# Optimization experiments

Measured on AMD Instinct MI355X. Metric: run time of the kernel, lower is better.

## Reference

```python
import jax, jax.numpy as jnp
import numpy as np

EPS = 1e-5
SCALE = 2
K_UP = 5


def _conv(x, w, pad):
    return jax.lax.conv_general_dilated(
        x, w, window_strides=(1, 1), padding=[(pad, pad), (pad, pad)],
        dimension_numbers=("NCHW", "OIHW", "NCHW"))


def _bn(x, gamma, beta, mean, var):
    scale = gamma / jnp.sqrt(var + EPS)
    return x * scale[None, :, None, None] + (beta - mean * scale)[None, :, None, None]


def _pixel_shuffle(x, r):
    b, cr2, h, w = x.shape
    c = cr2 // (r * r)
    x = x.reshape(b, c, r, r, h, w)
    x = x.transpose(0, 1, 4, 2, 5, 3)  # b, c, h, r, w, r
    return x.reshape(b, c, h * r, w * r)


def setup_inputs() -> dict:
    key = jax.random.key(0)
    ks = jax.random.split(key, 6)
    c, c_mid, k_enc = 256, 64, 3
    n_k = (SCALE * K_UP) ** 2  # 100
    return {
        "x": jax.random.normal(ks[0], (2, c, 64, 64), jnp.float32),
        "comp_w": jax.random.normal(ks[1], (c_mid, c, 1, 1), jnp.float32) * 0.05,
        "comp_gamma": jnp.ones((c_mid,), jnp.float32),
        "comp_beta": jnp.zeros((c_mid,), jnp.float32),
        "comp_mean": jax.random.normal(ks[2], (c_mid,), jnp.float32) * 0.1,
        "comp_var": jax.random.uniform(ks[3], (c_mid,), jnp.float32, 0.5, 1.5),
        "enc_w": jax.random.normal(ks[4], (n_k, c_mid, k_enc, k_enc), jnp.float32) * 0.05,
        "enc_gamma": jnp.ones((n_k,), jnp.float32),
        "enc_beta": jnp.zeros((n_k,), jnp.float32),
        "enc_mean": jax.random.normal(ks[5], (n_k,), jnp.float32) * 0.1,
        "enc_var": jnp.ones((n_k,), jnp.float32),
    }


def reference(x, comp_w, comp_gamma, comp_beta, comp_mean, comp_var,
              enc_w, enc_gamma, enc_beta, enc_mean, enc_var):
    b, c, h, w = x.shape
    h_, w_ = h * SCALE, w * SCALE
    # comp: 1x1 conv -> BN -> ReLU
    W = jax.nn.relu(_bn(_conv(x, comp_w, 0), comp_gamma, comp_beta, comp_mean, comp_var))
    # enc: 3x3 conv -> BN (no relu)
    W = _bn(_conv(W, enc_w, 1), enc_gamma, enc_beta, enc_mean, enc_var)
    # pixel shuffle to [b, k_up^2, h_, w_] then softmax over kernel dim
    W = _pixel_shuffle(W, SCALE)
    W = jax.nn.softmax(W, axis=1)
    # nearest upsample x2
    Xu = jnp.repeat(jnp.repeat(x, SCALE, axis=2), SCALE, axis=3)
    # unfold: kernel k_up, dilation=SCALE, padding=k_up//2*SCALE
    pad = (K_UP // 2) * SCALE
    Xp = jnp.pad(Xu, ((0, 0), (0, 0), (pad, pad), (pad, pad)))
    patches = jnp.stack(
        [Xp[:, :, i * SCALE:i * SCALE + h_, j * SCALE:j * SCALE + w_]
         for i in range(K_UP) for j in range(K_UP)], axis=2)  # [b,c,k^2,h_,w_]
    return jnp.einsum("bkhw,bckhw->bchw", W, patches)
```

## Files before the change

### kernel.cpp

```cpp
#include <hip/hip_runtime.h>
#include <hip/hip_bf16.h>

typedef __hip_bfloat16 bf16;
#define EPSF 1e-5f

__global__ void k1_comp(const float* __restrict__ x, const float* __restrict__ w,
                        const float* __restrict__ gamma, const float* __restrict__ beta,
                        const float* __restrict__ mean, const float* __restrict__ var,
                        float* __restrict__ comp) {
    __shared__ float shx[2][32 * 64];
    __shared__ float shw[256 * 20];
    const int pxt = blockIdx.x;
    const int ocg = blockIdx.y;
    const int b   = blockIdx.z;
    const int tid  = threadIdx.x;
    const int wave = tid >> 6, lane = tid & 63;
    const int oc0l = wave * 4;
    const int px0 = pxt << 6;
    const float* xb = x + b * (256 * 4096) + px0;

    const int f40 = tid * 2, f41 = tid * 2 + 1;
    const int r0 = f40 >> 4, c0 = f40 & 15;
    const int r1 = f41 >> 4, c1 = f41 & 15;

    float wtmp[16];
    #pragma unroll
    for (int k = 0; k < 16; ++k)
        wtmp[k] = w[(ocg * 16 + k) * 256 + tid];
    float4 xa = *(const float4*)(xb + r0 * 4096 + c0 * 4);
    float4 xc = *(const float4*)(xb + r1 * 4096 + c1 * 4);

    #pragma unroll
    for (int k = 0; k < 16; ++k)
        shw[tid * 20 + k] = wtmp[k];
    *(float4*)(&shx[0][r0 * 64 + c0 * 4]) = xa;
    *(float4*)(&shx[0][r1 * 64 + c1 * 4]) = xc;
    __syncthreads();

    float acc[4] = {0.f, 0.f, 0.f, 0.f};

    for (int icc = 0; icc < 8; ++icc) {
        const int buf = icc & 1;
        float4 na, nc;
        if (icc < 7) {
            na = *(const float4*)(xb + ((icc + 1) * 32 + r0) * 4096 + c0 * 4);
            nc = *(const float4*)(xb + ((icc + 1) * 32 + r1) * 4096 + c1 * 4);
        }
        #pragma unroll 8
        for (int ic_l = 0; ic_l < 32; ++ic_l) {
            float xv = shx[buf][ic_l * 64 + lane];
            float4 wv = *(const float4*)(&shw[(icc * 32 + ic_l) * 20 + oc0l]);
            acc[0] += xv * wv.x;
            acc[1] += xv * wv.y;
            acc[2] += xv * wv.z;
            acc[3] += xv * wv.w;
        }
        if (icc < 7) {
            *(float4*)(&shx[buf ^ 1][r0 * 64 + c0 * 4]) = na;
            *(float4*)(&shx[buf ^ 1][r1 * 64 + c1 * 4]) = nc;
        }
        __syncthreads();
    }
    #pragma unroll
    for (int m = 0; m < 4; ++m) {
        int mo = ocg * 16 + oc0l + m;
        float s = gamma[mo] * rsqrtf(var[mo] + EPSF);
        float r = acc[m] * s + (beta[mo] - mean[mo] * s);
        comp[(b * 64 + mo) * 4096 + px0 + lane] = fmaxf(r, 0.f);
    }
}

__global__ void k2_enc_part(const float* __restrict__ comp, const float* __restrict__ w,
                            float* __restrict__ encp) {
    __shared__ float sh[8 * 660];
    const int tile = blockIdx.x;
    const int og   = blockIdx.y >> 2;
    const int icc  = blockIdx.y & 3;
    const int b    = blockIdx.z;
    const int ty0 = tile << 3;
    const int tid = threadIdx.x;
    const int tx = tid & 31, ty = tid >> 5;
    const int o0 = og * 5;

    float accA[5], accB[5];
    #pragma unroll
    for (int i = 0; i < 5; ++i) { accA[i] = 0.f; accB[i] = 0.f; }

    for (int ics = 0; ics < 2; ++ics) {
        if (ics) __syncthreads();
        const float* cb = comp + (b * 64 + icc * 16 + ics * 8) * 4096;
        for (int idx = tid; idx < 8 * 660; idx += 256) {
            int ic_l = idx / 660;
            int rem  = idx - ic_l * 660;
            int r = rem / 66;
            int c = rem - r * 66;
            int gy = ty0 + r - 1;
            int gx = c - 1;
            float v = 0.f;
            if (gy >= 0 && gy < 64 && gx >= 0 && gx < 64)
                v = cb[(ic_l << 12) + (gy << 6) + gx];
            sh[ic_l * 660 + r * 66 + c] = v;
        }
        __syncthreads();

        #pragma unroll 2
        for (int ic_l = 0; ic_l < 8; ++ic_l) {
            const float* base = sh + ic_l * 660 + ty * 66 + 2 * tx;
            float t[3][4];
            #pragma unroll
            for (int dy = 0; dy < 3; ++dy)
                #pragma unroll
                for (int dx = 0; dx < 4; ++dx)
                    t[dy][dx] = base[dy * 66 + dx];
            const int ic = icc * 16 + ics * 8 + ic_l;
            #pragma unroll
            for (int o_l = 0; o_l < 5; ++o_l) {
                const float* wp = w + ((o0 + o_l) * 64 + ic) * 9;
                #pragma unroll
                for (int dy = 0; dy < 3; ++dy)
                    #pragma unroll
                    for (int dx = 0; dx < 3; ++dx) {
                        float wv = wp[dy * 3 + dx];
                        accA[o_l] += wv * t[dy][dx];
                        accB[o_l] += wv * t[dy][dx + 1];
                    }
            }
        }
    }
    const int pix = ((ty0 + ty) << 6) + 2 * tx;
    #pragma unroll
    for (int o_l = 0; o_l < 5; ++o_l) {
        float2 v = {accA[o_l], accB[o_l]};
        *(float2*)(&encp[((icc * 2 + b) * 100 + o0 + o_l) * 4096 + pix]) = v;
    }
}

__global__ void k3_softmax(const float* __restrict__ encp,
                           const float* __restrict__ gamma, const float* __restrict__ beta,
                           const float* __restrict__ mean, const float* __restrict__ var,
                           bf16* __restrict__ Wsm) {
    __shared__ float red[2][5][64];
    const int tid  = threadIdx.x;
    const int lane = tid & 63, wv = tid >> 6;
    const int item = blockIdx.x * 64 + lane;
    const int pos = item & 4095;
    const int g   = (item >> 12) & 3;
    const int b   = item >> 14;
    const int kbase = wv * 5;
    const size_t ICS = (size_t)200 * 4096;

    float L[5][4];
    #pragma unroll
    for (int q = 0; q < 5; ++q) {
        const int o = (kbase + q) * 4 + g;
        const float* ep = encp + ((size_t)b * 100 + o) * 4096 + pos;
        L[q][0] = ep[0];
        L[q][1] = ep[ICS];
        L[q][2] = ep[2 * ICS];
        L[q][3] = ep[3 * ICS];
    }
    float v[5];
    float mx = -1e30f;
    #pragma unroll
    for (int q = 0; q < 5; ++q) {
        const int o = (kbase + q) * 4 + g;
        float a = ((L[q][0] + L[q][1]) + L[q][2]) + L[q][3];
        float s = gamma[o] * rsqrtf(var[o] + EPSF);
        v[q] = a * s + (beta[o] - mean[o] * s);
        mx = fmaxf(mx, v[q]);
    }
    red[0][wv][lane] = mx;
    __syncthreads();
    mx = fmaxf(fmaxf(fmaxf(red[0][0][lane], red[0][1][lane]),
                     fmaxf(red[0][2][lane], red[0][3][lane])), red[0][4][lane]);
    float s = 0.f;
    #pragma unroll
    for (int q = 0; q < 5; ++q) { v[q] = __expf(v[q] - mx); s += v[q]; }
    red[1][wv][lane] = s;
    __syncthreads();
    s = (((red[1][0][lane] + red[1][1][lane]) + red[1][2][lane])
         + red[1][3][lane]) + red[1][4][lane];
    const float inv = 1.f / s;
    bf16* o_ = Wsm + ((size_t)(b * 4 + g) * 25 + kbase) * 4096 + pos;
    #pragma unroll
    for (int q = 0; q < 5; ++q) o_[q * 4096] = __float2bfloat16(v[q] * inv);
}

__global__ void k4_gather(const float* __restrict__ x, const bf16* __restrict__ Wsm,
                          float* __restrict__ out) {
    __shared__ float4 patch[8 * 36];
    const int tile   = blockIdx.x;
    const int cchunk = blockIdx.y;
    const int b      = blockIdx.z;
    const int ly0 = (tile >> 1) << 2;
    const int lx0 = (tile & 1) << 5;
    const int tid = threadIdx.x;
    const int ph = tid >> 7;
    const int r  = tid & 127;
    const int ly = r >> 5, lx = r & 31;
    const int yl = ly0 + ly, xl = lx0 + lx;

    float w0[25], w1[25];
    {
        const bf16* wp0 = Wsm + ((b * 4 + ph * 2    ) * 25) * 4096 + yl * 64 + xl;
        const bf16* wp1 = Wsm + ((b * 4 + ph * 2 + 1) * 25) * 4096 + yl * 64 + xl;
        #pragma unroll
        for (int k = 0; k < 25; ++k) {
            w0[k] = __bfloat162float(wp0[k * 4096]);
            w1[k] = __bfloat162float(wp1[k * 4096]);
        }
    }

    for (int cg = 0; cg < 2; ++cg) {
        const int c0 = cchunk * 8 + cg * 4;
        for (int idx = tid; idx < 8 * 36; idx += 256) {
            int pr = idx / 36, pc = idx - (idx / 36) * 36;
            int gy = ly0 - 2 + pr, gx = lx0 - 2 + pc;
            float4 v = {0.f, 0.f, 0.f, 0.f};
            if (gy >= 0 && gy < 64 && gx >= 0 && gx < 64) {
                const float* xp = x + ((b * 256 + c0) * 4096) + gy * 64 + gx;
                v.x = xp[0]; v.y = xp[4096]; v.z = xp[8192]; v.w = xp[12288];
            }
            patch[idx] = v;
        }
        __syncthreads();
        float4 a0 = {0.f, 0.f, 0.f, 0.f};
        float4 a1 = {0.f, 0.f, 0.f, 0.f};
        #pragma unroll
        for (int i = 0; i < 5; ++i) {
            #pragma unroll
            for (int j = 0; j < 5; ++j) {
                float4 xv = patch[(ly + i) * 36 + (lx + j)];
                float wa = w0[i * 5 + j], wb = w1[i * 5 + j];
                a0.x += wa * xv.x; a0.y += wa * xv.y; a0.z += wa * xv.z; a0.w += wa * xv.w;
                a1.x += wb * xv.x; a1.y += wb * xv.y; a1.z += wb * xv.z; a1.w += wb * xv.w;
            }
        }
        float* ob = out + (size_t)(b * 256 + c0) * 16384 + (2 * yl + ph) * 128 + 2 * xl;
        float2 s0 = {a0.x, a1.x}; *(float2*)(ob)           = s0;
        float2 s1 = {a0.y, a1.y}; *(float2*)(ob + 16384)   = s1;
        float2 s2 = {a0.z, a1.z}; *(float2*)(ob + 32768)   = s2;
        float2 s3 = {a0.w, a1.w}; *(float2*)(ob + 49152)   = s3;
        if (cg == 0) __syncthreads();
    }
}

extern "C" void kernel_launch(void* const* d_in, const int* in_sizes, int n_in,
                              void* d_out, int out_size, void* d_ws, size_t ws_size,
                              hipStream_t stream) {
    const float* x          = (const float*)d_in[0];
    const float* comp_w     = (const float*)d_in[1];
    const float* comp_gamma = (const float*)d_in[2];
    const float* comp_beta  = (const float*)d_in[3];
    const float* comp_mean  = (const float*)d_in[4];
    const float* comp_var   = (const float*)d_in[5];
    const float* enc_w      = (const float*)d_in[6];
    const float* enc_gamma  = (const float*)d_in[7];
    const float* enc_beta   = (const float*)d_in[8];
    const float* enc_mean   = (const float*)d_in[9];
    const float* enc_var    = (const float*)d_in[10];
    float* out = (float*)d_out;

    float* ws   = (float*)d_ws;
    float* comp = ws;
    float* encp = ws + 524288;
    bf16*  Wsm  = (bf16*)(ws + 524288 + 3276800);

    k1_comp<<<dim3(64, 4, 2), dim3(256), 0, stream>>>(x, comp_w, comp_gamma, comp_beta,
                                                      comp_mean, comp_var, comp);
    k2_enc_part<<<dim3(8, 80, 2), dim3(256), 0, stream>>>(comp, enc_w, encp);
    k3_softmax<<<dim3(512), dim3(320), 0, stream>>>(encp, enc_gamma, enc_beta,
                                                    enc_mean, enc_var, Wsm);
    k4_gather<<<dim3(32, 32, 2), dim3(256), 0, stream>>>(x, Wsm, out);
}
```

Before: 139.4 us.

## Prefetch next input tile into registers in enc conv and gather kernels

The enc conv kernel now loads the second channel batch into registers while computing on the first, then writes it to shared memory, so global latency overlaps compute. The gather kernel uses a double-buffered shared patch and processes 16 channels per block instead of 8. It prefetches the next 4-channel group during compute and halves the grid, which reuses the softmax weights loaded per thread across more channels. The cost is higher register pressure (21 staging registers plus 50 weights), which may lower occupancy.

```diff
diff --git a/kernel.cpp b/kernel.cpp
--- a/kernel.cpp
+++ b/kernel.cpp
@@ -81,28 +81,38 @@
     const int tid = threadIdx.x;
     const int tx = tid & 31, ty = tid >> 5;
     const int o0 = og * 5;
+    const float* cb = comp + (b * 64 + icc * 16) * 4096;
 
     float accA[5], accB[5];
     #pragma unroll
     for (int i = 0; i < 5; ++i) { accA[i] = 0.f; accB[i] = 0.f; }
 
-    for (int ics = 0; ics < 2; ++ics) {
-        if (ics) __syncthreads();
-        const float* cb = comp + (b * 64 + icc * 16 + ics * 8) * 4096;
-        for (int idx = tid; idx < 8 * 660; idx += 256) {
-            int ic_l = idx / 660;
-            int rem  = idx - ic_l * 660;
-            int r = rem / 66;
-            int c = rem - r * 66;
-            int gy = ty0 + r - 1;
-            int gx = c - 1;
+    auto load_batch = [&](int ics, float* tv) {
+        #pragma unroll
+        for (int k = 0; k < 21; ++k) {
+            int idx = tid + k * 256;
             float v = 0.f;
-            if (gy >= 0 && gy < 64 && gx >= 0 && gx < 64)
-                v = cb[(ic_l << 12) + (gy << 6) + gx];
-            sh[ic_l * 660 + r * 66 + c] = v;
-        }
-        __syncthreads();
-
+            if (idx < 5280) {
+                int ic_l = idx / 660;
+                int rem  = idx - ic_l * 660;
+                int r = rem / 66;
+                int c = rem - r * 66;
+                int gy = ty0 + r - 1;
+                int gx = c - 1;
+                if (gy >= 0 && gy < 64 && gx >= 0 && gx < 64)
+                    v = cb[((ics * 8 + ic_l) << 12) + (gy << 6) + gx];
+            }
+            tv[k] = v;
+        }
+    };
+    auto write_batch = [&](const float* tv) {
+        #pragma unroll
+        for (int k = 0; k < 21; ++k) {
+            int idx = tid + k * 256;
+            if (idx < 5280) sh[idx] = tv[k];
+        }
+    };
+    auto compute = [&](int ics) {
         #pragma unroll 2
         for (int ic_l = 0; ic_l < 8; ++ic_l) {
             const float* base = sh + ic_l * 660 + ty * 66 + 2 * tx;
@@ -126,7 +136,19 @@
                     }
             }
         }
-    }
+    };
+
+    float tv[21];
+    load_batch(0, tv);
+    write_batch(tv);
+    __syncthreads();
+    load_batch(1, tv);
+    compute(0);
+    __syncthreads();
+    write_batch(tv);
+    __syncthreads();
+    compute(1);
+
     const int pix = ((ty0 + ty) << 6) + 2 * tx;
     #pragma unroll
     for (int o_l = 0; o_l < 5; ++o_l) {
@@ -188,7 +210,7 @@
 
 __global__ void k4_gather(const float* __restrict__ x, const bf16* __restrict__ Wsm,
                           float* __restrict__ out) {
-    __shared__ float4 patch[8 * 36];
+    __shared__ float4 patch[2][8 * 36];
     const int tile   = blockIdx.x;
     const int cchunk = blockIdx.y;
     const int b      = blockIdx.z;
@@ -200,6 +222,27 @@
     const int ly = r >> 5, lx = r & 31;
     const int yl = ly0 + ly, xl = lx0 + lx;
 
+    const int pr0 = tid / 36, pc0 = tid - pr0 * 36;
+    const int pr1 = (tid + 256) / 36, pc1 = (tid + 256) - pr1 * 36;
+    const int gy0 = ly0 - 2 + pr0, gx0 = lx0 - 2 + pc0;
+    const int gy1 = ly0 - 2 + pr1, gx1 = lx0 - 2 + pc1;
+    const bool inb0 = (gy0 >= 0) && (gy0 < 64) && (gx0 >= 0) && (gx0 < 64);
+    const bool inb1 = (tid < 32) && (gy1 >= 0) && (gy1 < 64) && (gx1 >= 0) && (gx1 < 64);
+
+    auto ldpatch = [&](int cg, float4& v0, float4& v1) {
+        const int c0 = cchunk * 16 + cg * 4;
+        v0 = {0.f, 0.f, 0.f, 0.f};
+        v1 = {0.f, 0.f, 0.f, 0.f};
+        if (inb0) {
+            const float* xp = x + ((b * 256 + c0) * 4096) + gy0 * 64 + gx0;
+            v0.x = xp[0]; v0.y = xp[4096]; v0.z = xp[8192]; v0.w = xp[12288];
+        }
+        if (inb1) {
+            const float* xp = x + ((b * 256 + c0) * 4096) + gy1 * 64 + gx1;
+            v1.x = xp[0]; v1.y = xp[4096]; v1.z = xp[8192]; v1.w = xp[12288];
+        }
+    };
+
     float w0[25], w1[25];
     {
         const bf16* wp0 = Wsm + ((b * 4 + ph * 2    ) * 25) * 4096 + yl * 64 + xl;
@@ -211,37 +254,43 @@
         }
     }
 
-    for (int cg = 0; cg < 2; ++cg) {
-        const int c0 = cchunk * 8 + cg * 4;
-        for (int idx = tid; idx < 8 * 36; idx += 256) {
-            int pr = idx / 36, pc = idx - (idx / 36) * 36;
-            int gy = ly0 - 2 + pr, gx = lx0 - 2 + pc;
-            float4 v = {0.f, 0.f, 0.f, 0.f};
-            if (gy >= 0 && gy < 64 && gx >= 0 && gx < 64) {
-                const float* xp = x + ((b * 256 + c0) * 4096) + gy * 64 + gx;
-                v.x = xp[0]; v.y = xp[4096]; v.z = xp[8192]; v.w = xp[12288];
-            }
-            patch[idx] = v;
-        }
-        __syncthreads();
+    {
+        float4 s0, s1;
+        ldpatch(0, s0, s1);
+        patch[0][tid] = s0;
+        if (tid < 32) patch[0][tid + 256] = s1;
+    }
+    __syncthreads();
+
+    #pragma unroll
+    for (int cg = 0; cg < 4; ++cg) {
+        const int buf = cg & 1;
+        float4 n0, n1;
+        if (cg < 3) ldpatch(cg + 1, n0, n1);
         float4 a0 = {0.f, 0.f, 0.f, 0.f};
         float4 a1 = {0.f, 0.f, 0.f, 0.f};
+        const float4* pp = patch[buf];
         #pragma unroll
         for (int i = 0; i < 5; ++i) {
             #pragma unroll
             for (int j = 0; j < 5; ++j) {
-                float4 xv = patch[(ly + i) * 36 + (lx + j)];
+                float4 xv = pp[(ly + i) * 36 + (lx + j)];
                 float wa = w0[i * 5 + j], wb = w1[i * 5 + j];
                 a0.x += wa * xv.x; a0.y += wa * xv.y; a0.z += wa * xv.z; a0.w += wa * xv.w;
                 a1.x += wb * xv.x; a1.y += wb * xv.y; a1.z += wb * xv.z; a1.w += wb * xv.w;
             }
         }
+        if (cg < 3) {
+            patch[buf ^ 1][tid] = n0;
+            if (tid < 32) patch[buf ^ 1][tid + 256] = n1;
+        }
+        const int c0 = cchunk * 16 + cg * 4;
         float* ob = out + (size_t)(b * 256 + c0) * 16384 + (2 * yl + ph) * 128 + 2 * xl;
         float2 s0 = {a0.x, a1.x}; *(float2*)(ob)           = s0;
         float2 s1 = {a0.y, a1.y}; *(float2*)(ob + 16384)   = s1;
         float2 s2 = {a0.z, a1.z}; *(float2*)(ob + 32768)   = s2;
         float2 s3 = {a0.w, a1.w}; *(float2*)(ob + 49152)   = s3;
-        if (cg == 0) __syncthreads();
+        if (cg < 3) __syncthreads();
     }
 }
 
@@ -271,5 +320,5 @@
     k2_enc_part<<<dim3(8, 80, 2), dim3(256), 0, stream>>>(comp, enc_w, encp);
     k3_softmax<<<dim3(512), dim3(320), 0, stream>>>(encp, enc_gamma, enc_beta,
                                                     enc_mean, enc_var, Wsm);
-    k4_gather<<<dim3(32, 32, 2), dim3(256), 0, stream>>>(x, Wsm, out);
-}
+    k4_gather<<<dim3(32, 16, 2), dim3(256), 0, stream>>>(x, Wsm, out);
+}
```

After: 181.6 us. 1.3x slower.
